# Optimization experiments

Hardware: AMD Instinct MI355X
Metric: run time of the kernel (lower is better)

## Reference

```python
import jax, jax.numpy as jnp
import numpy as np

UNITS = 64        # rnn_cell.state_size
MOTOR = 4         # cell motor output dim (decoder input is 4)
ODE_UNFOLDS = 6
ELAPSED = 1.0
B, T, IN_DIM = 32, 512, 39


def setup_inputs() -> dict:
    ks = jax.random.split(jax.random.key(0), 32)
    gn = lambda k, s, sc: jax.random.normal(k, s, jnp.float32) * sc
    un = lambda k, s, lo, hi: jax.random.uniform(k, s, jnp.float32, lo, hi)
    sgn = lambda k, s: jnp.where(jax.random.normal(k, s) >= 0, 1.0, -1.0).astype(jnp.float32)
    inp = {}
    inp["x"] = jax.random.normal(ks[0], (B, T, IN_DIM), jnp.float32)
    # encoder MLP 39 -> 500 -> 500 -> 20 (weights stored [in, out])
    inp["enc_w0"] = gn(ks[1], (39, 500), 0.1);   inp["enc_b0"] = gn(ks[2], (500,), 0.01)
    inp["enc_w1"] = gn(ks[3], (500, 500), 0.04); inp["enc_b1"] = gn(ks[4], (500,), 0.01)
    inp["enc_w2"] = gn(ks[5], (500, 20), 0.04);  inp["enc_b2"] = gn(ks[6], (20,), 0.01)
    # decoder MLP 4 -> 500 -> 500 -> 30
    inp["dec_w0"] = gn(ks[7], (4, 500), 0.5);    inp["dec_b0"] = gn(ks[8], (500,), 0.01)
    inp["dec_w1"] = gn(ks[9], (500, 500), 0.04); inp["dec_b1"] = gn(ks[10], (500,), 0.01)
    inp["dec_w2"] = gn(ks[11], (500, 30), 0.04); inp["dec_b2"] = gn(ks[12], (30,), 0.01)
    # LTC cell parameters (ncps-style LTCCell, 20 sensory -> 64 units -> 4 motor)
    inp["gleak"] = un(ks[13], (UNITS,), 0.5, 1.5)
    inp["vleak"] = un(ks[14], (UNITS,), -0.2, 0.2)
    inp["cm"]    = un(ks[15], (UNITS,), 0.4, 0.6)
    inp["w"]     = un(ks[16], (UNITS, UNITS), 0.001, 1.0)
    inp["mu"]    = un(ks[17], (UNITS, UNITS), 0.3, 0.8)
    inp["sigma"] = un(ks[18], (UNITS, UNITS), 3.0, 8.0)
    inp["erev"]  = sgn(ks[19], (UNITS, UNITS))
    inp["sw"]    = un(ks[20], (20, UNITS), 0.001, 1.0)
    inp["smu"]   = un(ks[21], (20, UNITS), 0.3, 0.8)
    inp["ssigma"] = un(ks[22], (20, UNITS), 3.0, 8.0)
    inp["serev"] = sgn(ks[23], (20, UNITS))
    inp["in_w"]  = un(ks[24], (20,), 0.8, 1.2)
    inp["in_b"]  = gn(ks[25], (20,), 0.01)
    inp["out_w"] = un(ks[26], (MOTOR,), 0.8, 1.2)
    inp["out_b"] = gn(ks[27], (MOTOR,), 0.01)
    return inp


def reference(x, enc_w0, enc_b0, enc_w1, enc_b1, enc_w2, enc_b2,
              dec_w0, dec_b0, dec_w1, dec_b1, dec_w2, dec_b2,
              gleak, vleak, cm, w, mu, sigma, erev,
              sw, smu, ssigma, serev, in_w, in_b, out_w, out_b):
    # encoder MLP (tanh on hidden layers, linear last)
    h = jnp.tanh(x @ enc_w0 + enc_b0)
    h = jnp.tanh(h @ enc_w1 + enc_b1)
    h = h @ enc_w2 + enc_b2                      # [B, T, 20]

    cm_t = cm / (ELAPSED / ODE_UNFOLDS)

    def cell(v, u):                               # v: [B, 64], u: [B, 20]
        ui = u * in_w + in_b
        sa = sw * jax.nn.sigmoid((ui[:, :, None] - smu) * ssigma)   # [B, 20, 64]
        wnum_s = jnp.sum(sa * serev, axis=1)
        wden_s = jnp.sum(sa, axis=1)
        for _ in range(ODE_UNFOLDS):              # fixed small unroll (semi-implicit ODE)
            wa = w * jax.nn.sigmoid((v[:, :, None] - mu) * sigma)   # [B, 64, 64]
            wnum = jnp.sum(wa * erev, axis=1) + wnum_s
            wden = jnp.sum(wa, axis=1) + wden_s
            v = (cm_t * v + gleak * vleak + wnum) / (cm_t + gleak + wden + 1e-8)
        out = v[:, :MOTOR] * out_w + out_b        # motor readout [B, 4]
        return v, out

    v0 = jnp.zeros((x.shape[0], UNITS), x.dtype)
    _, outs = jax.lax.scan(cell, v0, jnp.swapaxes(h, 0, 1))  # outs: [T, B, 4]
    o = jnp.swapaxes(outs, 0, 1)                  # [B, T, 4]

    # decoder MLP
    o = jnp.tanh(o @ dec_w0 + dec_b0)
    o = jnp.tanh(o @ dec_w1 + dec_b1)
    return o @ dec_w2 + dec_b2                    # [B, T, 30]
```

## Files before the change

### kernel.cpp

```cpp
#include <hip/hip_runtime.h>
#include <cstdint>

typedef unsigned int uint;
typedef unsigned short ushort;

__device__ __forceinline__ float fexp2(float x) { return __builtin_amdgcn_exp2f(x); }
__device__ __forceinline__ float frcp(float x)  { return __builtin_amdgcn_rcpf(x); }

__device__ __forceinline__ float fast_tanh(float x) {
    x = fminf(15.0f, fmaxf(-15.0f, x));
    float E = fexp2(x * 2.8853900817779268f);
    float d = E + 1.0f;
    float r = frcp(d);
    r = r * (2.0f - d * r);
    return (E - 1.0f) * r;
}

__device__ __forceinline__ ushort f2bf(float x) {
    uint u = __float_as_uint(x);
    return (ushort)((u + 0x7fffu + ((u >> 16) & 1u)) >> 16);
}
__device__ __forceinline__ uint pk2bf(float lo, float hi) {
    return (uint)f2bf(lo) | ((uint)f2bf(hi) << 16);
}

#define BM 64
#define BN 64
#define BK 16

template<bool TANH>
__global__ __launch_bounds__(256) void gemm_bias(
    const float* __restrict__ A, const float* __restrict__ W,
    const float* __restrict__ bias, float* __restrict__ C,
    int M, int N, int K)
{
    __shared__ float As[BK][BM + 4];
    __shared__ float Bs[BK][BN + 4];

    const int tid = threadIdx.x;
    const int tx = tid & 15;
    const int ty = tid >> 4;
    const int m0 = blockIdx.y * BM;
    const int n0 = blockIdx.x * BN;

    float acc[4][4] = {};

    for (int k0 = 0; k0 < K; k0 += BK) {
        #pragma unroll
        for (int ld = 0; ld < 4; ++ld) {
            int e  = tid + ld * 256;
            int kk = e & 15, mm = e >> 4;
            int kg = k0 + kk;
            As[kk][mm] = (kg < K) ? A[(size_t)(m0 + mm) * K + kg] : 0.0f;
        }
        #pragma unroll
        for (int ld = 0; ld < 4; ++ld) {
            int e  = tid + ld * 256;
            int nn = e & 63, kk = e >> 6;
            int kg = k0 + kk, ng = n0 + nn;
            Bs[kk][nn] = (kg < K && ng < N) ? W[(size_t)kg * N + ng] : 0.0f;
        }
        __syncthreads();

        #pragma unroll
        for (int kk = 0; kk < BK; ++kk) {
            float4 a  = *(const float4*)&As[kk][ty * 4];
            float4 bq = *(const float4*)&Bs[kk][tx * 4];
            float av[4] = {a.x, a.y, a.z, a.w};
            float bv[4] = {bq.x, bq.y, bq.z, bq.w};
            #pragma unroll
            for (int i2 = 0; i2 < 4; ++i2)
                #pragma unroll
                for (int j2 = 0; j2 < 4; ++j2)
                    acc[i2][j2] += av[i2] * bv[j2];
        }
        __syncthreads();
    }

    const int cbase = n0 + tx * 4;
    if (cbase >= N) return;

    float bb[4];
    if (cbase + 3 < N) {
        float4 b4 = *(const float4*)&bias[cbase];
        bb[0] = b4.x; bb[1] = b4.y; bb[2] = b4.z; bb[3] = b4.w;
    } else {
        #pragma unroll
        for (int e = 0; e < 4; ++e) bb[e] = (cbase + e < N) ? bias[cbase + e] : 0.0f;
    }

    #pragma unroll
    for (int i2 = 0; i2 < 4; ++i2) {
        int row = m0 + ty * 4 + i2;
        float o[4];
        #pragma unroll
        for (int j2 = 0; j2 < 4; ++j2) {
            float v = acc[i2][j2] + bb[j2];
            o[j2] = TANH ? fast_tanh(v) : v;
        }
        if (cbase + 3 < N) {
            float4 o4 = {o[0], o[1], o[2], o[3]};
            *(float4*)&C[(size_t)row * N + cbase] = o4;
        } else {
            #pragma unroll
            for (int j2 = 0; j2 < 4; ++j2)
                if (cbase + j2 < N) C[(size_t)row * N + cbase + j2] = o[j2];
        }
    }
}

__global__ __launch_bounds__(256) void wt_pad(
    const float* __restrict__ W, ushort* __restrict__ out, int K, int N)
{
    int idx = blockIdx.x * 256 + threadIdx.x;
    int n = idx >> 9, k = idx & 511;
    float v = (n < N && k < K) ? W[(size_t)k * N + n] : 0.0f;
    out[idx] = f2bf(v);
}

typedef __attribute__((ext_vector_type(8))) short bf16x8;
typedef __attribute__((ext_vector_type(4))) float f32x4;

template<bool TANH>
__global__ __launch_bounds__(256) void mfma_gemm(
    const float* __restrict__ A, const ushort* __restrict__ Wt,
    const float* __restrict__ bias, float* __restrict__ C,
    int M, int N)
{
    __shared__ ushort As[128][40];
    __shared__ ushort Bs[128][40];

    const int tid = threadIdx.x;
    const int l   = tid & 63;
    const int wv  = tid >> 6;
    const int wr  = wv >> 1, wc = wv & 1;
    const int m0  = blockIdx.y * 128;
    const int n0  = blockIdx.x * 128;

    const int srow = tid >> 1;
    const int shalf = tid & 1;

    const int fr = l & 15;
    const int ko = l >> 4;

    f32x4 acc[4][4];
    #pragma unroll
    for (int i = 0; i < 4; ++i)
        #pragma unroll
        for (int j = 0; j < 4; ++j) acc[i][j] = (f32x4){0.f, 0.f, 0.f, 0.f};

    const float* Arow = A + (size_t)(m0 + srow) * 500;
    const ushort* Wrow = Wt + (size_t)(n0 + srow) * 512;

    for (int kc = 0; kc < 512; kc += 32) {
        {
            int kb = kc + shalf * 16;
            float4 v0 = (kb +  3 < 500) ? *(const float4*)(Arow + kb)      : (float4){0,0,0,0};
            float4 v1 = (kb +  7 < 500) ? *(const float4*)(Arow + kb + 4)  : (float4){0,0,0,0};
            float4 v2 = (kb + 11 < 500) ? *(const float4*)(Arow + kb + 8)  : (float4){0,0,0,0};
            float4 v3 = (kb + 15 < 500) ? *(const float4*)(Arow + kb + 12) : (float4){0,0,0,0};
            uint4 p0 = {pk2bf(v0.x, v0.y), pk2bf(v0.z, v0.w), pk2bf(v1.x, v1.y), pk2bf(v1.z, v1.w)};
            uint4 p1 = {pk2bf(v2.x, v2.y), pk2bf(v2.z, v2.w), pk2bf(v3.x, v3.y), pk2bf(v3.z, v3.w)};
            *(uint4*)&As[srow][shalf * 16]     = p0;
            *(uint4*)&As[srow][shalf * 16 + 8] = p1;
            uint4 b0 = *(const uint4*)(Wrow + kc + shalf * 16);
            uint4 b1 = *(const uint4*)(Wrow + kc + shalf * 16 + 8);
            *(uint4*)&Bs[srow][shalf * 16]     = b0;
            *(uint4*)&Bs[srow][shalf * 16 + 8] = b1;
        }
        __syncthreads();

        bf16x8 af[4], bf[4];
        #pragma unroll
        for (int mi = 0; mi < 4; ++mi)
            af[mi] = *(const bf16x8*)&As[wr * 64 + mi * 16 + fr][ko * 8];
        #pragma unroll
        for (int ni = 0; ni < 4; ++ni)
            bf[ni] = *(const bf16x8*)&Bs[wc * 64 + ni * 16 + fr][ko * 8];

        #pragma unroll
        for (int mi = 0; mi < 4; ++mi)
            #pragma unroll
            for (int ni = 0; ni < 4; ++ni)
                acc[mi][ni] = __builtin_amdgcn_mfma_f32_16x16x32_bf16(
                    af[mi], bf[ni], acc[mi][ni], 0, 0, 0);
        __syncthreads();
    }

    #pragma unroll
    for (int mi = 0; mi < 4; ++mi) {
        #pragma unroll
        for (int ni = 0; ni < 4; ++ni) {
            int col = n0 + wc * 64 + ni * 16 + fr;
            if (col >= N) continue;
            float bb = bias[col];
            #pragma unroll
            for (int r = 0; r < 4; ++r) {
                int row = m0 + wr * 64 + mi * 16 + ko * 4 + r;
                float v = acc[mi][ni][r] + bb;
                C[(size_t)row * N + col] = TANH ? fast_tanh(v) : v;
            }
        }
    }
}

__global__ __launch_bounds__(256) void dec_l1(
    const float* __restrict__ Mo, const float* __restrict__ Wd,
    const float* __restrict__ bd, float* __restrict__ O)
{
    int idx = blockIdx.x * 256 + threadIdx.x;
    int r  = idx / 125;
    int c4 = (idx % 125) * 4;
    float4 m = *(const float4*)&Mo[(size_t)r * 4];
    float4 w0 = *(const float4*)&Wd[0 * 500 + c4];
    float4 w1 = *(const float4*)&Wd[1 * 500 + c4];
    float4 w2 = *(const float4*)&Wd[2 * 500 + c4];
    float4 w3 = *(const float4*)&Wd[3 * 500 + c4];
    float4 b  = *(const float4*)&bd[c4];
    float o0 = b.x + m.x * w0.x + m.y * w1.x + m.z * w2.x + m.w * w3.x;
    float o1 = b.y + m.x * w0.y + m.y * w1.y + m.z * w2.y + m.w * w3.y;
    float o2 = b.z + m.x * w0.z + m.y * w1.z + m.z * w2.z + m.w * w3.z;
    float o3 = b.w + m.x * w0.w + m.y * w1.w + m.z * w2.w + m.w * w3.w;
    float4 o = {fast_tanh(o0), fast_tanh(o1), fast_tanh(o2), fast_tanh(o3)};
    *(float4*)&O[(size_t)r * 500 + c4] = o;
}

#define SEQ_T 512

__global__ __launch_bounds__(512, 2) void ltc_scan(
    const float* __restrict__ h,
    const float* __restrict__ gleak, const float* __restrict__ vleak,
    const float* __restrict__ cm,
    const float* __restrict__ w,  const float* __restrict__ mu,
    const float* __restrict__ sg, const float* __restrict__ erev,
    const float* __restrict__ sw,  const float* __restrict__ smu,
    const float* __restrict__ ssg, const float* __restrict__ serev,
    const float* __restrict__ in_w, const float* __restrict__ in_b,
    const float* __restrict__ out_w, const float* __restrict__ out_b,
    float* __restrict__ motor)
{
    const int b   = blockIdx.x;
    const int tid = threadIdx.x;
    const int w8  = tid >> 6;
    const int l   = tid & 63;
    const int jl  = l & 7;
    const int ig  = l >> 3;
    const int j   = 8 * w8 + jl;

    const float LOG2E = 1.4426950408889634f;

    __shared__ float vbuf[2][64];

    float A1[8], B1[8], Wp[8], WE[8];
    #pragma unroll
    for (int r = 0; r < 8; ++r) {
        int i = 8 * ig + r;
        float s = sg[i * 64 + j];
        A1[r] = s * LOG2E;
        B1[r] = mu[i * 64 + j] * s * LOG2E;
        Wp[r] = w[i * 64 + j];
        WE[r] = Wp[r] * erev[i * 64 + j];
    }
    float sA[3], sB[3], sWp[3], sWE[3], uw[3], ub[3];
    int   sI[3];
    #pragma unroll
    for (int r = 0; r < 3; ++r) {
        int i = ig + 8 * r;
        bool live = (i < 20);
        sI[r] = live ? i : 0;
        float s = ssg[sI[r] * 64 + j];
        sA[r]  = s * LOG2E;
        sB[r]  = smu[sI[r] * 64 + j] * s * LOG2E;
        sWp[r] = live ? sw[sI[r] * 64 + j] : 0.0f;
        sWE[r] = live ? sWp[r] * serev[sI[r] * 64 + j] : 0.0f;
        uw[r]  = in_w[sI[r]];
        ub[r]  = in_b[sI[r]];
    }

    const float cmt  = cm[j] * 6.0f;
    const float gl   = gleak[j];
    const float glvl = gl * vleak[j];
    const float gle  = cmt + gl + 1e-8f;
    const float ow   = out_w[j & 3], ob = out_b[j & 3];

    float vj = 0.0f;
    const float* hb = h + (size_t)b * SEQ_T * 20;
    float* mb = motor + (size_t)b * SEQ_T * 4;

    float u_cur[3], u_nxt[3];
    #pragma unroll
    for (int r = 0; r < 3; ++r) u_cur[r] = hb[sI[r]];

    if (tid < 64) vbuf[0][tid] = 0.0f;
    __syncthreads();

    int cur = 0;
    for (int t = 0; t < SEQ_T; ++t) {
        int tn = (t + 1 < SEQ_T) ? (t + 1) : t;
        #pragma unroll
        for (int r = 0; r < 3; ++r) u_nxt[r] = hb[tn * 20 + sI[r]];

        float ns = 0.0f, ds = 0.0f;
        #pragma unroll
        for (int r = 0; r < 3; ++r) {
            float ui = fmaf(u_cur[r], uw[r], ub[r]);
            float x  = sB[r] - ui * sA[r];
            float E  = fexp2(x);
            float s  = frcp(1.0f + E);
            ns = fmaf(sWE[r], s, ns);
            ds = fmaf(sWp[r], s, ds);
        }
        ns += __shfl_xor(ns, 8);  ds += __shfl_xor(ds, 8);
        ns += __shfl_xor(ns, 16); ds += __shfl_xor(ds, 16);
        ns += __shfl_xor(ns, 32); ds += __shfl_xor(ds, 32);

        #pragma unroll 1
        for (int uf = 0; uf < 6; ++uf) {
            float4 va = *(const float4*)&vbuf[cur][8 * ig];
            float4 vc = *(const float4*)&vbuf[cur][8 * ig + 4];
            float vv[8] = {va.x, va.y, va.z, va.w, vc.x, vc.y, vc.z, vc.w};

            float an = 0.0f, ad = 0.0f;
            #pragma unroll
            for (int r = 0; r < 8; ++r) {
                float x = fmaf(-vv[r], A1[r], B1[r]);
                float E = fexp2(x);
                float s = frcp(1.0f + E);
                an = fmaf(WE[r], s, an);
                ad = fmaf(Wp[r], s, ad);
            }
            an += __shfl_xor(an, 8);  ad += __shfl_xor(ad, 8);
            an += __shfl_xor(an, 16); ad += __shfl_xor(ad, 16);
            an += __shfl_xor(an, 32); ad += __shfl_xor(ad, 32);

            float num = fmaf(cmt, vj, glvl) + an + ns;
            float den = gle + ad + ds;
            vj = num * frcp(den);

            if (ig == 0) vbuf[cur ^ 1][j] = vj;
            __syncthreads();
            cur ^= 1;
        }

        if (w8 == 0 && ig == 0 && jl < 4) mb[t * 4 + jl] = fmaf(vj, ow, ob);

        #pragma unroll
        for (int r = 0; r < 3; ++r) u_cur[r] = u_nxt[r];
    }
}

extern "C" void kernel_launch(void* const* d_in, const int* in_sizes, int n_in,
                              void* d_out, int out_size, void* d_ws, size_t ws_size,
                              hipStream_t stream) {
    const float* x      = (const float*)d_in[0];
    const float* enc_w0 = (const float*)d_in[1];
    const float* enc_b0 = (const float*)d_in[2];
    const float* enc_w1 = (const float*)d_in[3];
    const float* enc_b1 = (const float*)d_in[4];
    const float* enc_w2 = (const float*)d_in[5];
    const float* enc_b2 = (const float*)d_in[6];
    const float* dec_w0 = (const float*)d_in[7];
    const float* dec_b0 = (const float*)d_in[8];
    const float* dec_w1 = (const float*)d_in[9];
    const float* dec_b1 = (const float*)d_in[10];
    const float* dec_w2 = (const float*)d_in[11];
    const float* dec_b2 = (const float*)d_in[12];
    const float* gleak  = (const float*)d_in[13];
    const float* vleak  = (const float*)d_in[14];
    const float* cm     = (const float*)d_in[15];
    const float* w      = (const float*)d_in[16];
    const float* mu     = (const float*)d_in[17];
    const float* sigma  = (const float*)d_in[18];
    const float* erev   = (const float*)d_in[19];
    const float* sw     = (const float*)d_in[20];
    const float* smu    = (const float*)d_in[21];
    const float* ssigma = (const float*)d_in[22];
    const float* serev  = (const float*)d_in[23];
    const float* in_w   = (const float*)d_in[24];
    const float* in_b   = (const float*)d_in[25];
    const float* out_w  = (const float*)d_in[26];
    const float* out_b  = (const float*)d_in[27];

    float* ws   = (float*)d_ws;
    float* buf1 = ws;
    float* buf2 = ws + 8192000;
    float* hbuf = ws + 16384000;
    float* mbuf = ws + 16711680;
    ushort* Wt  = (ushort*)hbuf;

    dim3 blk(256);
    wt_pad<<<dim3(1024), blk, 0, stream>>>(enc_w1, Wt, 500, 500);
    gemm_bias<true ><<<dim3(8, 256), blk, 0, stream>>>(x, enc_w0, enc_b0, buf1, 16384, 500, 39);
    mfma_gemm<true ><<<dim3(4, 128), blk, 0, stream>>>(buf1, Wt, enc_b1, buf2, 16384, 500);
    gemm_bias<false><<<dim3(1, 256), blk, 0, stream>>>(buf2, enc_w2, enc_b2, hbuf, 16384, 20, 500);
    ltc_scan<<<dim3(32), dim3(512), 0, stream>>>(hbuf, gleak, vleak, cm, w, mu, sigma, erev,
                                                 sw, smu, ssigma, serev, in_w, in_b, out_w, out_b, mbuf);
    wt_pad<<<dim3(1024), blk, 0, stream>>>(dec_w1, Wt, 500, 500);
    dec_l1<<<dim3(8000), blk, 0, stream>>>(mbuf, dec_w0, dec_b0, buf1);
    mfma_gemm<true ><<<dim3(4, 128), blk, 0, stream>>>(buf1, Wt, dec_b1, buf2, 16384, 500);
    gemm_bias<false><<<dim3(1, 256), blk, 0, stream>>>(buf2, dec_w2, dec_b2, (float*)d_out, 16384, 30, 500);
}
```

Before: 1.876 ms.

## Move encoder layers 0 and 2 to bf16 MFMA and use DPP/permlane reductions

Encoder layer 0 (K=39) and layer 2 (N=20) now run on bf16 MFMA kernels instead of the scalar fp32 tiled GEMM. All three encoder weight matrices are transposed and padded in one prep kernel. The LTC scan's cross-lane reductions switch from shuffles to DPP row-shuffle and permlane32 swap where available, which shortens the serial recurrence. Trade-offs: bf16 rounding on the first and last encoder layers, an extra prep kernel, and a bias-load path in gemm_bias that is now always scalar.

After: 1.689 ms. -10.0%, faster.

```diff
diff --git a/kernel.cpp b/kernel.cpp
--- a/kernel.cpp
+++ b/kernel.cpp
@@ -24,6 +24,22 @@
     return (uint)f2bf(lo) | ((uint)f2bf(hi) << 16);
 }
 
+__device__ __forceinline__ float bfly8(float x) {
+    float t = __uint_as_float(__builtin_amdgcn_update_dpp(
+        0, (int)__float_as_uint(x), 0x128, 0xf, 0xf, true));
+    return x + t;
+}
+__device__ __forceinline__ float bfly32(float x) {
+#if __has_builtin(__builtin_amdgcn_permlane32_swap)
+    typedef unsigned int uv2 __attribute__((ext_vector_type(2)));
+    uv2 r = __builtin_amdgcn_permlane32_swap(
+        __float_as_uint(x), __float_as_uint(x), false, false);
+    return __uint_as_float(r.x) + __uint_as_float(r.y);
+#else
+    return x + __shfl_xor(x, 32);
+#endif
+}
+
 #define BM 64
 #define BN 64
 #define BK 16
@@ -81,13 +97,8 @@
     if (cbase >= N) return;
 
     float bb[4];
-    if (cbase + 3 < N) {
-        float4 b4 = *(const float4*)&bias[cbase];
-        bb[0] = b4.x; bb[1] = b4.y; bb[2] = b4.z; bb[3] = b4.w;
-    } else {
-        #pragma unroll
-        for (int e = 0; e < 4; ++e) bb[e] = (cbase + e < N) ? bias[cbase + e] : 0.0f;
-    }
+    #pragma unroll
+    for (int e = 0; e < 4; ++e) bb[e] = (cbase + e < N) ? bias[cbase + e] : 0.0f;
 
     #pragma unroll
     for (int i2 = 0; i2 < 4; ++i2) {
@@ -106,6 +117,26 @@
             for (int j2 = 0; j2 < 4; ++j2)
                 if (cbase + j2 < N) C[(size_t)row * N + cbase + j2] = o[j2];
         }
+    }
+}
+
+__global__ __launch_bounds__(256) void prep1(
+    const float* __restrict__ w0, const float* __restrict__ w1,
+    const float* __restrict__ w2,
+    ushort* __restrict__ Wt1e, ushort* __restrict__ Wt0e, ushort* __restrict__ Wt2e)
+{
+    int idx = blockIdx.x * 256 + threadIdx.x;
+    if (idx < 262144) {
+        int n = idx >> 9, k = idx & 511;
+        Wt1e[idx] = f2bf((n < 500 && k < 500) ? w1[(size_t)k * 500 + n] : 0.0f);
+    } else if (idx < 294912) {
+        int i = idx - 262144;
+        int n = i >> 6, k = i & 63;
+        Wt0e[i] = f2bf((n < 500 && k < 39) ? w0[(size_t)k * 500 + n] : 0.0f);
+    } else {
+        int i = idx - 294912;
+        int n = i >> 9, k = i & 511;
+        Wt2e[i] = f2bf((n < 20 && k < 500) ? w2[(size_t)k * 20 + n] : 0.0f);
     }
 }
 
@@ -204,6 +235,167 @@
     }
 }
 
+template<bool TANH>
+__global__ __launch_bounds__(256) void mfma_gemm_k64(
+    const float* __restrict__ A, const ushort* __restrict__ Wt,
+    const float* __restrict__ bias, float* __restrict__ C,
+    int M, int N, int KA)
+{
+    __shared__ ushort As[128][40];
+    __shared__ ushort Bs[128][40];
+
+    const int tid = threadIdx.x;
+    const int l   = tid & 63;
+    const int wv  = tid >> 6;
+    const int wr  = wv >> 1, wc = wv & 1;
+    const int m0  = blockIdx.y * 128;
+    const int n0  = blockIdx.x * 128;
+
+    const int srow = tid >> 1;
+    const int shalf = tid & 1;
+    const int fr = l & 15;
+    const int ko = l >> 4;
+
+    f32x4 acc[4][4];
+    #pragma unroll
+    for (int i = 0; i < 4; ++i)
+        #pragma unroll
+        for (int j = 0; j < 4; ++j) acc[i][j] = (f32x4){0.f, 0.f, 0.f, 0.f};
+
+    const float* Arow = A + (size_t)(m0 + srow) * KA;
+    const ushort* Wrow = Wt + (size_t)(n0 + srow) * 64;
+
+    for (int kc = 0; kc < 64; kc += 32) {
+        {
+            int kb = kc + shalf * 16;
+            uint pk[8];
+            #pragma unroll
+            for (int e = 0; e < 8; ++e) {
+                int k2 = kb + 2 * e;
+                float lo = (k2     < KA) ? Arow[k2]     : 0.0f;
+                float hi = (k2 + 1 < KA) ? Arow[k2 + 1] : 0.0f;
+                pk[e] = pk2bf(lo, hi);
+            }
+            *(uint4*)&As[srow][shalf * 16]     = *(uint4*)&pk[0];
+            *(uint4*)&As[srow][shalf * 16 + 8] = *(uint4*)&pk[4];
+            *(uint4*)&Bs[srow][shalf * 16]     = *(const uint4*)(Wrow + kc + shalf * 16);
+            *(uint4*)&Bs[srow][shalf * 16 + 8] = *(const uint4*)(Wrow + kc + shalf * 16 + 8);
+        }
+        __syncthreads();
+
+        bf16x8 af[4], bf[4];
+        #pragma unroll
+        for (int mi = 0; mi < 4; ++mi)
+            af[mi] = *(const bf16x8*)&As[wr * 64 + mi * 16 + fr][ko * 8];
+        #pragma unroll
+        for (int ni = 0; ni < 4; ++ni)
+            bf[ni] = *(const bf16x8*)&Bs[wc * 64 + ni * 16 + fr][ko * 8];
+
+        #pragma unroll
+        for (int mi = 0; mi < 4; ++mi)
+            #pragma unroll
+            for (int ni = 0; ni < 4; ++ni)
+                acc[mi][ni] = __builtin_amdgcn_mfma_f32_16x16x32_bf16(
+                    af[mi], bf[ni], acc[mi][ni], 0, 0, 0);
+        __syncthreads();
+    }
+
+    #pragma unroll
+    for (int mi = 0; mi < 4; ++mi) {
+        #pragma unroll
+        for (int ni = 0; ni < 4; ++ni) {
+            int col = n0 + wc * 64 + ni * 16 + fr;
+            if (col >= N) continue;
+            float bb = bias[col];
+            #pragma unroll
+            for (int r = 0; r < 4; ++r) {
+                int row = m0 + wr * 64 + mi * 16 + ko * 4 + r;
+                float v = acc[mi][ni][r] + bb;
+                C[(size_t)row * N + col] = TANH ? fast_tanh(v) : v;
+            }
+        }
+    }
+}
+
+__global__ __launch_bounds__(256) void mfma_gemm_n32(
+    const float* __restrict__ A, const ushort* __restrict__ Wt,
+    const float* __restrict__ bias, float* __restrict__ C,
+    int M, int N)
+{
+    __shared__ ushort As[128][40];
+    __shared__ ushort Bs[32][40];
+
+    const int tid = threadIdx.x;
+    const int l   = tid & 63;
+    const int wv  = tid >> 6;
+    const int m0  = blockIdx.y * 128;
+
+    const int srow = tid >> 1;
+    const int shalf = tid & 1;
+    const int fr = l & 15;
+    const int ko = l >> 4;
+
+    f32x4 acc[2][2];
+    #pragma unroll
+    for (int i = 0; i < 2; ++i)
+        #pragma unroll
+        for (int j = 0; j < 2; ++j) acc[i][j] = (f32x4){0.f, 0.f, 0.f, 0.f};
+
+    const float* Arow = A + (size_t)(m0 + srow) * 500;
+
+    for (int kc = 0; kc < 512; kc += 32) {
+        {
+            int kb = kc + shalf * 16;
+            float4 v0 = (kb +  3 < 500) ? *(const float4*)(Arow + kb)      : (float4){0,0,0,0};
+            float4 v1 = (kb +  7 < 500) ? *(const float4*)(Arow + kb + 4)  : (float4){0,0,0,0};
+            float4 v2 = (kb + 11 < 500) ? *(const float4*)(Arow + kb + 8)  : (float4){0,0,0,0};
+            float4 v3 = (kb + 15 < 500) ? *(const float4*)(Arow + kb + 12) : (float4){0,0,0,0};
+            uint4 p0 = {pk2bf(v0.x, v0.y), pk2bf(v0.z, v0.w), pk2bf(v1.x, v1.y), pk2bf(v1.z, v1.w)};
+            uint4 p1 = {pk2bf(v2.x, v2.y), pk2bf(v2.z, v2.w), pk2bf(v3.x, v3.y), pk2bf(v3.z, v3.w)};
+            *(uint4*)&As[srow][shalf * 16]     = p0;
+            *(uint4*)&As[srow][shalf * 16 + 8] = p1;
+            if (tid < 64) {
+                int br = tid >> 1, bh = tid & 1;
+                const ushort* Wr = Wt + (size_t)br * 512 + kc + bh * 16;
+                *(uint4*)&Bs[br][bh * 16]     = *(const uint4*)(Wr);
+                *(uint4*)&Bs[br][bh * 16 + 8] = *(const uint4*)(Wr + 8);
+            }
+        }
+        __syncthreads();
+
+        bf16x8 af[2], bf[2];
+        #pragma unroll
+        for (int mi = 0; mi < 2; ++mi)
+            af[mi] = *(const bf16x8*)&As[wv * 32 + mi * 16 + fr][ko * 8];
+        #pragma unroll
+        for (int ni = 0; ni < 2; ++ni)
+            bf[ni] = *(const bf16x8*)&Bs[ni * 16 + fr][ko * 8];
+
+        #pragma unroll
+        for (int mi = 0; mi < 2; ++mi)
+            #pragma unroll
+            for (int ni = 0; ni < 2; ++ni)
+                acc[mi][ni] = __builtin_amdgcn_mfma_f32_16x16x32_bf16(
+                    af[mi], bf[ni], acc[mi][ni], 0, 0, 0);
+        __syncthreads();
+    }
+
+    #pragma unroll
+    for (int mi = 0; mi < 2; ++mi) {
+        #pragma unroll
+        for (int ni = 0; ni < 2; ++ni) {
+            int col = ni * 16 + fr;
+            if (col >= N) continue;
+            float bb = bias[col];
+            #pragma unroll
+            for (int r = 0; r < 4; ++r) {
+                int row = m0 + wv * 32 + mi * 16 + ko * 4 + r;
+                C[(size_t)row * N + col] = acc[mi][ni][r] + bb;
+            }
+        }
+    }
+}
+
 __global__ __launch_bounds__(256) void dec_l1(
     const float* __restrict__ Mo, const float* __restrict__ Wd,
     const float* __restrict__ bd, float* __restrict__ O)
@@ -310,9 +502,9 @@
             ns = fmaf(sWE[r], s, ns);
             ds = fmaf(sWp[r], s, ds);
         }
-        ns += __shfl_xor(ns, 8);  ds += __shfl_xor(ds, 8);
+        ns = bfly8(ns);  ds = bfly8(ds);
         ns += __shfl_xor(ns, 16); ds += __shfl_xor(ds, 16);
-        ns += __shfl_xor(ns, 32); ds += __shfl_xor(ds, 32);
+        ns = bfly32(ns); ds = bfly32(ds);
 
         #pragma unroll 1
         for (int uf = 0; uf < 6; ++uf) {
@@ -329,9 +521,9 @@
                 an = fmaf(WE[r], s, an);
                 ad = fmaf(Wp[r], s, ad);
             }
-            an += __shfl_xor(an, 8);  ad += __shfl_xor(ad, 8);
+            an = bfly8(an);  ad = bfly8(ad);
             an += __shfl_xor(an, 16); ad += __shfl_xor(ad, 16);
-            an += __shfl_xor(an, 32); ad += __shfl_xor(ad, 32);
+            an = bfly32(an); ad = bfly32(ad);
 
             float num = fmaf(cmt, vj, glvl) + an + ns;
             float den = gle + ad + ds;
@@ -386,17 +578,22 @@
     float* buf2 = ws + 8192000;
     float* hbuf = ws + 16384000;
     float* mbuf = ws + 16711680;
-    ushort* Wt  = (ushort*)hbuf;
+
+    ushort* hb16 = (ushort*)hbuf;
+    ushort* Wt1e = hb16;
+    ushort* Wt0e = hb16 + 262144;
+    ushort* Wt2e = (ushort*)mbuf;
+    ushort* Wt1d = hb16;
 
     dim3 blk(256);
-    wt_pad<<<dim3(1024), blk, 0, stream>>>(enc_w1, Wt, 500, 500);
-    gemm_bias<true ><<<dim3(8, 256), blk, 0, stream>>>(x, enc_w0, enc_b0, buf1, 16384, 500, 39);
-    mfma_gemm<true ><<<dim3(4, 128), blk, 0, stream>>>(buf1, Wt, enc_b1, buf2, 16384, 500);
-    gemm_bias<false><<<dim3(1, 256), blk, 0, stream>>>(buf2, enc_w2, enc_b2, hbuf, 16384, 20, 500);
+    prep1<<<dim3(1216), blk, 0, stream>>>(enc_w0, enc_w1, enc_w2, Wt1e, Wt0e, Wt2e);
+    mfma_gemm_k64<true><<<dim3(4, 128), blk, 0, stream>>>(x, Wt0e, enc_b0, buf1, 16384, 500, 39);
+    mfma_gemm<true><<<dim3(4, 128), blk, 0, stream>>>(buf1, Wt1e, enc_b1, buf2, 16384, 500);
+    mfma_gemm_n32<<<dim3(1, 128), blk, 0, stream>>>(buf2, Wt2e, enc_b2, hbuf, 16384, 20);
     ltc_scan<<<dim3(32), dim3(512), 0, stream>>>(hbuf, gleak, vleak, cm, w, mu, sigma, erev,
                                                  sw, smu, ssigma, serev, in_w, in_b, out_w, out_b, mbuf);
-    wt_pad<<<dim3(1024), blk, 0, stream>>>(dec_w1, Wt, 500, 500);
+    wt_pad<<<dim3(1024), blk, 0, stream>>>(dec_w1, Wt1d, 500, 500);
     dec_l1<<<dim3(8000), blk, 0, stream>>>(mbuf, dec_w0, dec_b0, buf1);
-    mfma_gemm<true ><<<dim3(4, 128), blk, 0, stream>>>(buf1, Wt, dec_b1, buf2, 16384, 500);
+    mfma_gemm<true><<<dim3(4, 128), blk, 0, stream>>>(buf1, Wt1d, dec_b1, buf2, 16384, 500);
     gemm_bias<false><<<dim3(1, 256), blk, 0, stream>>>(buf2, dec_w2, dec_b2, (float*)d_out, 16384, 30, 500);
 }
```
